# Optimization experiments

Hardware: AMD Instinct MI355X
Metric: run time of the kernel (lower is better)

Reference implementation:

```python
import jax, jax.numpy as jnp
import numpy as np

B, T, C, H = 4, 2048, 1024, 16
NEG = -1e9  # masked-fill value (finite to keep grads clean)


def setup_inputs() -> dict:
    key = jax.random.key(0)
    ks = jax.random.split(key, 5)
    s = 1.0 / np.sqrt(C)  # keep logits O(1) like trained linear layers
    return {
        "x": jax.random.normal(ks[0], (B, T, C), dtype=jnp.float32),
        "wq": jax.random.normal(ks[1], (C, C), dtype=jnp.float32) * s,
        "bq": jnp.zeros((C,), dtype=jnp.float32),
        "wk": jax.random.normal(ks[2], (C, C), dtype=jnp.float32) * s,
        "bk": jnp.zeros((C,), dtype=jnp.float32),
        "wv": jax.random.normal(ks[3], (C, C), dtype=jnp.float32) * s,
        "bv": jnp.zeros((C,), dtype=jnp.float32),
        "wo": jax.random.normal(ks[4], (C, C), dtype=jnp.float32) * s,
        "bo": jnp.zeros((C,), dtype=jnp.float32),
    }


def _split_heads(y):
    # [B,T,C] -> [B,H,T,hd]
    b, t, c = y.shape
    return y.reshape(b, t, H, c // H).transpose(0, 2, 1, 3)


def reference(x, wq, bq, wk, bk, wv, bv, wo, bo):
    b, t, c = x.shape
    scale = (c // H) ** (-0.5)
    q = _split_heads(x @ wq.T + bq)  # [B,H,T,hd]
    k = _split_heads(x @ wk.T + bk)
    v = _split_heads(x @ wv.T + bv)
    att = jnp.einsum("bhqd,bhkd->bhqk", q, k) * scale  # [B,H,T,T]
    causal = jnp.tril(jnp.ones((t, t), dtype=bool))
    att = jnp.where(causal[None, None], att, NEG)
    att = jax.nn.softmax(att, axis=-1)  # dropout is identity in eval mode
    y = jnp.einsum("bhqk,bhkd->bhqd", att, v)
    y = y.transpose(0, 2, 1, 3).reshape(b, t, c)
    return y @ wo.T + bo
```

## Files before the change

kernel.cpp:

```cpp
#include <hip/hip_runtime.h>


#define B_ 4
#define T_ 2048
#define C_ 1024
#define H_ 16
#define M_ 8192

typedef unsigned short u16;
typedef __bf16 bf16x8 __attribute__((ext_vector_type(8)));
typedef float f32x4 __attribute__((ext_vector_type(4)));

static __device__ __forceinline__ u16 f2bf(float f) {
  unsigned int u = __float_as_uint(f);
  u += 0x7fffu + ((u >> 16) & 1u);
  return (u16)(u >> 16);
}

static __device__ __forceinline__ void async16(const void* g, void* l) {
  __builtin_amdgcn_global_load_lds(
      (const __attribute__((address_space(1))) unsigned int*)g,
      (__attribute__((address_space(3))) unsigned int*)l, 16, 0, 0);
}

#if __has_builtin(__builtin_amdgcn_exp2f)
#define EXP2F(x) __builtin_amdgcn_exp2f(x)
#else
#define EXP2F(x) exp2f(x)
#endif

static __device__ __forceinline__ f32x4 mfma32(bf16x8 a, bf16x8 b, f32x4 c) {
  return __builtin_amdgcn_mfma_f32_16x16x32_bf16(a, b, c, 0, 0, 0);
}

__global__ __launch_bounds__(256) void cvt_x(const float* __restrict__ src,
                                             u16* __restrict__ dst, int n4) {
  int i = blockIdx.x * 256 + threadIdx.x;
  if (i >= n4) return;
  float4 f = ((const float4*)src)[i];
  ushort4 o;
  o.x = f2bf(f.x); o.y = f2bf(f.y); o.z = f2bf(f.z); o.w = f2bf(f.w);
  ((ushort4*)dst)[i] = o;
}

__global__ __launch_bounds__(256) void cvt_w4(const float* __restrict__ w0,
                                              const float* __restrict__ w1,
                                              const float* __restrict__ w2,
                                              const float* __restrict__ w3,
                                              u16* __restrict__ o0, u16* __restrict__ o1,
                                              u16* __restrict__ o2, u16* __restrict__ o3,
                                              float s0) {
  int i = blockIdx.x * 256 + threadIdx.x;
  const float* src; u16* dst; float s = 1.f;
  switch (blockIdx.y) {
    case 0: src = w0; dst = o0; s = s0; break;
    case 1: src = w1; dst = o1; break;
    case 2: src = w2; dst = o2; break;
    default: src = w3; dst = o3; break;
  }
  float4 f = ((const float4*)src)[i];
  ushort4 o;
  o.x = f2bf(f.x * s); o.y = f2bf(f.y * s); o.z = f2bf(f.z * s); o.w = f2bf(f.w * s);
  ((ushort4*)dst)[i] = o;
}

__global__ __launch_bounds__(256) void gemm_bt(const u16* __restrict__ A,
                                               const u16* __restrict__ Bt,
                                               const float* __restrict__ bias,
                                               float bscale,
                                               float* __restrict__ outf,
                                               u16* __restrict__ outb,
                                               u16* __restrict__ outbT,
                                               int M, int N, int K) {
  __shared__ __align__(16) u16 Asm[128 * 32];
  __shared__ __align__(16) u16 Bsm[128 * 32];
  const int tid = threadIdx.x, lane = tid & 63, wave = tid >> 6;
  const int quad = lane >> 4, l16 = lane & 15;
  const int wm = wave >> 1, wn = wave & 1;
  const int row0 = blockIdx.y * 128, col0 = blockIdx.x * 128;

  f32x4 zero = {0.f, 0.f, 0.f, 0.f};
  f32x4 acc[4][4];
#pragma unroll
  for (int i = 0; i < 4; i++)
#pragma unroll
    for (int j = 0; j < 4; j++) acc[i][j] = zero;

  for (int k0 = 0; k0 < K; k0 += 32) {
#pragma unroll
    for (int i = 0; i < 2; i++) {
      int c = wave * 128 + i * 64 + lane;
      int r = c >> 2;
      int gcc = (c & 3) ^ (r & 3);
      async16(A + (size_t)(row0 + r) * K + k0 + gcc * 8,
              Asm + (size_t)(wave * 128 + i * 64) * 8);
      async16(Bt + (size_t)(col0 + r) * K + k0 + gcc * 8,
              Bsm + (size_t)(wave * 128 + i * 64) * 8);
    }
    __syncthreads();

    bf16x8 a[4], b[4];
#pragma unroll
    for (int i = 0; i < 4; i++) {
      int rm = wm * 64 + 16 * i + l16;
      a[i] = *(const bf16x8*)(Asm + rm * 32 + (quad ^ (rm & 3)) * 8);
      int rn = wn * 64 + 16 * i + l16;
      b[i] = *(const bf16x8*)(Bsm + rn * 32 + (quad ^ (rn & 3)) * 8);
    }
#pragma unroll
    for (int i = 0; i < 4; i++)
#pragma unroll
      for (int j = 0; j < 4; j++)
        acc[i][j] = mfma32(a[i], b[j], acc[i][j]);
    __syncthreads();
  }

  float bj[4];
#pragma unroll
  for (int j = 0; j < 4; j++) bj[j] = bias[col0 + wn * 64 + 16 * j + l16] * bscale;
#pragma unroll
  for (int i = 0; i < 4; i++) {
#pragma unroll
    for (int j = 0; j < 4; j++) {
      int gcol = col0 + wn * 64 + 16 * j + l16;
      int grow0 = row0 + wm * 64 + 16 * i + quad * 4;
      if (outbT) {
        int d = gcol & 63, hh = gcol >> 6;
        int bb = grow0 >> 11, t0 = grow0 & 2047;
        union { u16 s[4]; uint2 u; } w;
#pragma unroll
        for (int r = 0; r < 4; r++) w.s[r] = f2bf(acc[i][j][r] + bj[j]);
        *(uint2*)(outbT + ((size_t)((bb * 16 + hh) * 64 + d)) * T_ + t0) = w.u;
      } else {
#pragma unroll
        for (int r = 0; r < 4; r++) {
          int grow = grow0 + r;
          float v = acc[i][j][r] + bj[j];
          if (outf) outf[(size_t)grow * N + gcol] = v;
          else outb[(size_t)grow * N + gcol] = f2bf(v);
        }
      }
    }
  }
}

__global__ __launch_bounds__(256) void attn(const u16* __restrict__ q,
                                            const u16* __restrict__ k,
                                            const u16* __restrict__ vt,
                                            u16* __restrict__ y) {
  __shared__ __align__(16) u16 Ksm[64 * 64];
  __shared__ __align__(16) u16 Vsm[64 * 64];
  __shared__ __align__(16) u16 Psm[4][32 * 64];
  const int tid = threadIdx.x, lane = tid & 63, wave = tid >> 6;
  const int quad = lane >> 4, l16 = lane & 15;
  static const int qperm[16] = {15, 14, 11, 10, 12, 13, 8, 9, 3, 2, 7, 6, 0, 1, 4, 5};
  const int bh = blockIdx.x;
  const int qt = qperm[blockIdx.y];
  const int b = bh >> 4, h = bh & 15;
  const int jtN = 2 * qt + 2;
  const int jt_d = 2 * qt + (wave >> 1);

  bf16x8 qf[2][2];
#pragma unroll
  for (int m = 0; m < 2; m++) {
    const u16* qp =
        q + (size_t)(b * T_ + qt * 128 + wave * 32 + m * 16 + l16) * C_ + h * 64;
#pragma unroll
    for (int ks = 0; ks < 2; ks++)
      qf[m][ks] = *(const bf16x8*)(qp + ks * 32 + quad * 8);
  }

  f32x4 zero = {0.f, 0.f, 0.f, 0.f};
  f32x4 o[2][4];
  float lp[2][4];
#pragma unroll
  for (int m = 0; m < 2; m++) {
#pragma unroll
    for (int dt = 0; dt < 4; dt++) o[m][dt] = zero;
#pragma unroll
    for (int r = 0; r < 4; r++) lp[m][r] = 0.f;
  }

  const u16* kp[2];
  const u16* vp[2];
#pragma unroll
  for (int i = 0; i < 2; i++) {
    int c = i * 256 + tid;
    int r = c >> 3, lc = (c & 7) ^ (r & 7);
    kp[i] = k + (size_t)(b * T_ + r) * C_ + h * 64 + lc * 8;
    vp[i] = vt + (size_t)(bh * 64 + r) * T_ + lc * 8;
  }

  int qrel[2];
#pragma unroll
  for (int m = 0; m < 2; m++)
    qrel[m] = wave * 32 + m * 16 + quad * 4 - (wave >> 1) * 64 - l16;
  const int nlim0 = 2 * (wave & 1) + 1;

  u16* Pw = &Psm[wave][0];

#pragma unroll 1
  for (int jt = 0; jt < jtN; ++jt) {
#pragma unroll
    for (int i = 0; i < 2; i++) {
      async16(kp[i], Ksm + (size_t)(i * 256 + wave * 64) * 8);
      async16(vp[i], Vsm + (size_t)(i * 256 + wave * 64) * 8);
      kp[i] += (size_t)64 * C_;
      vp[i] += 64;
    }
    __syncthreads();

    if (jt <= jt_d) {
      const bool diag = (jt == jt_d);
#pragma unroll
      for (int n = 0; n < 4; ++n) {
        int rk = n * 16 + l16;
        bf16x8 kf0 = *(const bf16x8*)(Ksm + rk * 64 + ((quad ^ (rk & 7)) * 8));
        bf16x8 kf1 = *(const bf16x8*)(Ksm + rk * 64 + (((4 + quad) ^ (rk & 7)) * 8));
#pragma unroll
        for (int m = 0; m < 2; ++m) {
          if (!diag || n < nlim0 + m) {
            f32x4 s = mfma32(qf[m][0], kf0, zero);
            s = mfma32(qf[m][1], kf1, s);
            float e[4];
#pragma unroll
            for (int r = 0; r < 4; r++) e[r] = EXP2F(s[r]);
            if (diag) {
              int rmin = n * 16 - qrel[m];
#pragma unroll
              for (int r = 0; r < 4; r++)
                if (r < rmin) e[r] = 0.f;
            }
#pragma unroll
            for (int r = 0; r < 4; r++) {
              lp[m][r] += e[r];
              int qr = m * 16 + quad * 4 + r;
              Pw[qr * 64 + (((n * 2 + (l16 >> 3)) ^ (qr & 7)) * 8) + (l16 & 7)] =
                  f2bf(e[r]);
            }
          } else {
#pragma unroll
            for (int r = 0; r < 4; r++) {
              int qr = m * 16 + quad * 4 + r;
              Pw[qr * 64 + (((n * 2 + (l16 >> 3)) ^ (qr & 7)) * 8) + (l16 & 7)] = 0;
            }
          }
        }
      }
      bf16x8 pf[2][2];
#pragma unroll
      for (int m = 0; m < 2; m++)
#pragma unroll
        for (int ks = 0; ks < 2; ks++)
          pf[m][ks] = *(const bf16x8*)(Pw + (m * 16 + l16) * 64 +
                                       (((ks * 4 + quad) ^ (l16 & 7)) * 8));
#pragma unroll
      for (int dt = 0; dt < 4; ++dt) {
        int rv = dt * 16 + l16;
        bf16x8 vf0 = *(const bf16x8*)(Vsm + rv * 64 + ((quad ^ (rv & 7)) * 8));
        bf16x8 vf1 = *(const bf16x8*)(Vsm + rv * 64 + (((4 + quad) ^ (rv & 7)) * 8));
#pragma unroll
        for (int m = 0; m < 2; m++) {
          o[m][dt] = mfma32(pf[m][0], vf0, o[m][dt]);
          o[m][dt] = mfma32(pf[m][1], vf1, o[m][dt]);
        }
      }
    }
    __syncthreads();
  }

#pragma unroll
  for (int m = 0; m < 2; m++)
#pragma unroll
    for (int r = 0; r < 4; r++) {
      float v = lp[m][r];
      v += __shfl_xor(v, 1);
      v += __shfl_xor(v, 2);
      v += __shfl_xor(v, 4);
      v += __shfl_xor(v, 8);
      lp[m][r] = 1.f / v;
    }

#pragma unroll
  for (int m = 0; m < 2; m++)
#pragma unroll
    for (int r = 0; r < 4; r++) {
      int grow = b * T_ + qt * 128 + wave * 32 + m * 16 + quad * 4 + r;
#pragma unroll
      for (int dt = 0; dt < 4; dt++)
        y[(size_t)grow * C_ + h * 64 + dt * 16 + l16] = f2bf(o[m][dt][r] * lp[m][r]);
    }
}

extern "C" void kernel_launch(void* const* d_in, const int* in_sizes, int n_in,
                              void* d_out, int out_size, void* d_ws, size_t ws_size,
                              hipStream_t stream) {
  const float* x  = (const float*)d_in[0];
  const float* wq = (const float*)d_in[1];
  const float* bq = (const float*)d_in[2];
  const float* wk = (const float*)d_in[3];
  const float* bk = (const float*)d_in[4];
  const float* wv = (const float*)d_in[5];
  const float* bv = (const float*)d_in[6];
  const float* wo = (const float*)d_in[7];
  const float* bo = (const float*)d_in[8];
  float* out = (float*)d_out;

  const float QSCALE = 0.125f * 1.4426950408889634f;

  u16* xb  = (u16*)d_ws;
  u16* wqb = xb  + (size_t)M_ * C_;
  u16* wkb = wqb + (size_t)C_ * C_;
  u16* wvb = wkb + (size_t)C_ * C_;
  u16* wob = wvb + (size_t)C_ * C_;
  u16* qb  = wob + (size_t)C_ * C_;
  u16* kb  = qb  + (size_t)M_ * C_;
  u16* vtb = kb  + (size_t)M_ * C_;
  u16* yb  = xb;

  cvt_x<<<M_ * C_ / 4 / 256, 256, 0, stream>>>(x, xb, M_ * C_ / 4);
  cvt_w4<<<dim3(C_ * C_ / 4 / 256, 4), 256, 0, stream>>>(
      wq, wk, wv, wo, wqb, wkb, wvb, wob, QSCALE);

  dim3 gg(C_ / 128, M_ / 128);
  gemm_bt<<<gg, 256, 0, stream>>>(xb, wqb, bq, QSCALE, nullptr, qb, nullptr,
                                  M_, C_, C_);
  gemm_bt<<<gg, 256, 0, stream>>>(xb, wkb, bk, 1.f, nullptr, kb, nullptr,
                                  M_, C_, C_);
  gemm_bt<<<gg, 256, 0, stream>>>(xb, wvb, bv, 1.f, nullptr, nullptr, vtb,
                                  M_, C_, C_);

  attn<<<dim3(B_ * H_, 16), 256, 0, stream>>>(qb, kb, vtb, yb);

  gemm_bt<<<gg, 256, 0, stream>>>(yb, wob, bo, 1.f, out, nullptr, nullptr,
                                  M_, C_, C_);
}
```

Before: 311.3 us.

## Fuse QKV projections into one launch and deepen GEMM K-tile to 64

```diff
diff --git a/kernel.cpp b/kernel.cpp
--- a/kernel.cpp
+++ b/kernel.cpp
@@ -64,20 +64,24 @@
   ((ushort4*)dst)[i] = o;
 }
 
-__global__ __launch_bounds__(256) void gemm_bt(const u16* __restrict__ A,
-                                               const u16* __restrict__ Bt,
-                                               const float* __restrict__ bias,
-                                               float bscale,
-                                               float* __restrict__ outf,
-                                               u16* __restrict__ outb,
-                                               u16* __restrict__ outbT,
-                                               int M, int N, int K) {
-  __shared__ __align__(16) u16 Asm[128 * 32];
-  __shared__ __align__(16) u16 Bsm[128 * 32];
+__global__ __launch_bounds__(256) void gemm_qkv(const u16* __restrict__ A,
+                                                const u16* __restrict__ W,
+                                                const float* __restrict__ bq,
+                                                const float* __restrict__ bk,
+                                                const float* __restrict__ bv,
+                                                float qscale,
+                                                u16* __restrict__ outqk,
+                                                u16* __restrict__ vtb) {
+  __shared__ __align__(16) u16 Asm[128 * 64];
+  __shared__ __align__(16) u16 Bsm[128 * 64];
   const int tid = threadIdx.x, lane = tid & 63, wave = tid >> 6;
   const int quad = lane >> 4, l16 = lane & 15;
   const int wm = wave >> 1, wn = wave & 1;
-  const int row0 = blockIdx.y * 128, col0 = blockIdx.x * 128;
+  const int sel = blockIdx.x >> 3;
+  const int col0 = (blockIdx.x & 7) * 128, row0 = blockIdx.y * 128;
+  const u16* Bt = W + (size_t)sel * C_ * C_;
+  const float* bias = sel == 0 ? bq : (sel == 1 ? bk : bv);
+  const float bscale = sel == 0 ? qscale : 1.f;
 
   f32x4 zero = {0.f, 0.f, 0.f, 0.f};
   f32x4 acc[4][4];
@@ -86,32 +90,34 @@
 #pragma unroll
     for (int j = 0; j < 4; j++) acc[i][j] = zero;
 
-  for (int k0 = 0; k0 < K; k0 += 32) {
-#pragma unroll
-    for (int i = 0; i < 2; i++) {
-      int c = wave * 128 + i * 64 + lane;
-      int r = c >> 2;
-      int gcc = (c & 3) ^ (r & 3);
-      async16(A + (size_t)(row0 + r) * K + k0 + gcc * 8,
-              Asm + (size_t)(wave * 128 + i * 64) * 8);
-      async16(Bt + (size_t)(col0 + r) * K + k0 + gcc * 8,
-              Bsm + (size_t)(wave * 128 + i * 64) * 8);
-    }
-    __syncthreads();
-
-    bf16x8 a[4], b[4];
+  for (int k0 = 0; k0 < C_; k0 += 64) {
 #pragma unroll
     for (int i = 0; i < 4; i++) {
-      int rm = wm * 64 + 16 * i + l16;
-      a[i] = *(const bf16x8*)(Asm + rm * 32 + (quad ^ (rm & 3)) * 8);
-      int rn = wn * 64 + 16 * i + l16;
-      b[i] = *(const bf16x8*)(Bsm + rn * 32 + (quad ^ (rn & 3)) * 8);
-    }
-#pragma unroll
-    for (int i = 0; i < 4; i++)
-#pragma unroll
-      for (int j = 0; j < 4; j++)
-        acc[i][j] = mfma32(a[i], b[j], acc[i][j]);
+      int c = i * 256 + tid;
+      int r = c >> 3, gcc = (c & 7) ^ (r & 7);
+      async16(A + (size_t)(row0 + r) * C_ + k0 + gcc * 8,
+              Asm + (size_t)(i * 256 + wave * 64) * 8);
+      async16(Bt + (size_t)(col0 + r) * C_ + k0 + gcc * 8,
+              Bsm + (size_t)(i * 256 + wave * 64) * 8);
+    }
+    __syncthreads();
+
+#pragma unroll
+    for (int kk = 0; kk < 2; kk++) {
+      bf16x8 a[4], b[4];
+#pragma unroll
+      for (int i = 0; i < 4; i++) {
+        int rm = wm * 64 + 16 * i + l16;
+        a[i] = *(const bf16x8*)(Asm + rm * 64 + (((kk * 4 + quad) ^ (rm & 7)) * 8));
+        int rn = wn * 64 + 16 * i + l16;
+        b[i] = *(const bf16x8*)(Bsm + rn * 64 + (((kk * 4 + quad) ^ (rn & 7)) * 8));
+      }
+#pragma unroll
+      for (int i = 0; i < 4; i++)
+#pragma unroll
+        for (int j = 0; j < 4; j++)
+          acc[i][j] = mfma32(a[i], b[j], acc[i][j]);
+    }
     __syncthreads();
   }
 
@@ -124,22 +130,84 @@
     for (int j = 0; j < 4; j++) {
       int gcol = col0 + wn * 64 + 16 * j + l16;
       int grow0 = row0 + wm * 64 + 16 * i + quad * 4;
-      if (outbT) {
+      if (sel == 2) {
         int d = gcol & 63, hh = gcol >> 6;
         int bb = grow0 >> 11, t0 = grow0 & 2047;
         union { u16 s[4]; uint2 u; } w;
 #pragma unroll
         for (int r = 0; r < 4; r++) w.s[r] = f2bf(acc[i][j][r] + bj[j]);
-        *(uint2*)(outbT + ((size_t)((bb * 16 + hh) * 64 + d)) * T_ + t0) = w.u;
+        *(uint2*)(vtb + ((size_t)((bb * 16 + hh) * 64 + d)) * T_ + t0) = w.u;
       } else {
-#pragma unroll
-        for (int r = 0; r < 4; r++) {
-          int grow = grow0 + r;
-          float v = acc[i][j][r] + bj[j];
-          if (outf) outf[(size_t)grow * N + gcol] = v;
-          else outb[(size_t)grow * N + gcol] = f2bf(v);
-        }
-      }
+        u16* dst = outqk + (size_t)sel * M_ * C_;
+#pragma unroll
+        for (int r = 0; r < 4; r++)
+          dst[(size_t)(grow0 + r) * C_ + gcol] = f2bf(acc[i][j][r] + bj[j]);
+      }
+    }
+  }
+}
+
+__global__ __launch_bounds__(256) void gemm_o(const u16* __restrict__ A,
+                                              const u16* __restrict__ Bt,
+                                              const float* __restrict__ bias,
+                                              float* __restrict__ outf) {
+  __shared__ __align__(16) u16 Asm[128 * 64];
+  __shared__ __align__(16) u16 Bsm[128 * 64];
+  const int tid = threadIdx.x, lane = tid & 63, wave = tid >> 6;
+  const int quad = lane >> 4, l16 = lane & 15;
+  const int wm = wave >> 1, wn = wave & 1;
+  const int col0 = blockIdx.x * 128, row0 = blockIdx.y * 128;
+
+  f32x4 zero = {0.f, 0.f, 0.f, 0.f};
+  f32x4 acc[4][4];
+#pragma unroll
+  for (int i = 0; i < 4; i++)
+#pragma unroll
+    for (int j = 0; j < 4; j++) acc[i][j] = zero;
+
+  for (int k0 = 0; k0 < C_; k0 += 64) {
+#pragma unroll
+    for (int i = 0; i < 4; i++) {
+      int c = i * 256 + tid;
+      int r = c >> 3, gcc = (c & 7) ^ (r & 7);
+      async16(A + (size_t)(row0 + r) * C_ + k0 + gcc * 8,
+              Asm + (size_t)(i * 256 + wave * 64) * 8);
+      async16(Bt + (size_t)(col0 + r) * C_ + k0 + gcc * 8,
+              Bsm + (size_t)(i * 256 + wave * 64) * 8);
+    }
+    __syncthreads();
+
+#pragma unroll
+    for (int kk = 0; kk < 2; kk++) {
+      bf16x8 a[4], b[4];
+#pragma unroll
+      for (int i = 0; i < 4; i++) {
+        int rm = wm * 64 + 16 * i + l16;
+        a[i] = *(const bf16x8*)(Asm + rm * 64 + (((kk * 4 + quad) ^ (rm & 7)) * 8));
+        int rn = wn * 64 + 16 * i + l16;
+        b[i] = *(const bf16x8*)(Bsm + rn * 64 + (((kk * 4 + quad) ^ (rn & 7)) * 8));
+      }
+#pragma unroll
+      for (int i = 0; i < 4; i++)
+#pragma unroll
+        for (int j = 0; j < 4; j++)
+          acc[i][j] = mfma32(a[i], b[j], acc[i][j]);
+    }
+    __syncthreads();
+  }
+
+  float bj[4];
+#pragma unroll
+  for (int j = 0; j < 4; j++) bj[j] = bias[col0 + wn * 64 + 16 * j + l16];
+#pragma unroll
+  for (int i = 0; i < 4; i++) {
+#pragma unroll
+    for (int j = 0; j < 4; j++) {
+      int gcol = col0 + wn * 64 + 16 * j + l16;
+      int grow0 = row0 + wm * 64 + 16 * i + quad * 4;
+#pragma unroll
+      for (int r = 0; r < 4; r++)
+        outf[(size_t)(grow0 + r) * C_ + gcol] = acc[i][j][r] + bj[j];
     }
   }
 }
@@ -322,16 +390,10 @@
   cvt_w4<<<dim3(C_ * C_ / 4 / 256, 4), 256, 0, stream>>>(
       wq, wk, wv, wo, wqb, wkb, wvb, wob, QSCALE);
 
-  dim3 gg(C_ / 128, M_ / 128);
-  gemm_bt<<<gg, 256, 0, stream>>>(xb, wqb, bq, QSCALE, nullptr, qb, nullptr,
-                                  M_, C_, C_);
-  gemm_bt<<<gg, 256, 0, stream>>>(xb, wkb, bk, 1.f, nullptr, kb, nullptr,
-                                  M_, C_, C_);
-  gemm_bt<<<gg, 256, 0, stream>>>(xb, wvb, bv, 1.f, nullptr, nullptr, vtb,
-                                  M_, C_, C_);
+  gemm_qkv<<<dim3(24, M_ / 128), 256, 0, stream>>>(xb, wqb, bq, bk, bv, QSCALE,
+                                                   qb, vtb);
 
   attn<<<dim3(B_ * H_, 16), 256, 0, stream>>>(qb, kb, vtb, yb);
 
-  gemm_bt<<<gg, 256, 0, stream>>>(yb, wob, bo, 1.f, out, nullptr, nullptr,
-                                  M_, C_, C_);
-}
+  gemm_o<<<dim3(C_ / 128, M_ / 128), 256, 0, stream>>>(yb, wob, bo, out);
+}
```

After: 272.4 us. 12.5% less time.
